# Performance work log

Hardware: AMD Instinct MI355X
Metric: run time of the kernel (lower is better)

Reference implementation:

```python
import jax, jax.numpy as jnp
import numpy as np

HIDDEN = 1024
HEADS = 16
HEAD_DIM = HIDDEN // HEADS


def setup_inputs() -> dict:
    key = jax.random.key(0)
    ks = jax.random.split(key, 7)
    B, S = 2, 2048
    scale = 1.0 / np.sqrt(HIDDEN)
    return {
        "hidden_states": jax.random.normal(ks[0], (B, S, HIDDEN), dtype=jnp.float32),
        "attention_mask": jnp.zeros((B, S), dtype=jnp.float32),
        "Wq": jax.random.normal(ks[1], (HIDDEN, HIDDEN), dtype=jnp.float32) * scale,
        "bq": jnp.zeros((HIDDEN,), dtype=jnp.float32),
        "Wk": jax.random.normal(ks[2], (HIDDEN, HIDDEN), dtype=jnp.float32) * scale,
        "bk": jnp.zeros((HIDDEN,), dtype=jnp.float32),
        "Wv": jax.random.normal(ks[3], (HIDDEN, HIDDEN), dtype=jnp.float32) * scale,
        "bv": jnp.zeros((HIDDEN,), dtype=jnp.float32),
    }


def reference(hidden_states, attention_mask, Wq, bq, Wk, bk, Wv, bv):
    B, S, _ = hidden_states.shape
    def heads(x):  # [B,S,HIDDEN] -> [B,H,S,D]
        return x.reshape(B, S, HEADS, HEAD_DIM).transpose(0, 2, 1, 3)
    q = heads(hidden_states @ Wq + bq)
    k = heads(hidden_states @ Wk + bk)
    v = heads(hidden_states @ Wv + bv)
    scores = jnp.einsum('bhqd,bhkd->bhqk', q, k) / np.sqrt(HEAD_DIM).astype(np.float32)
    # additive mask broadcast [B,1,1,S]
    scores = scores + attention_mask[:, None, None, :]
    probs = jax.nn.softmax(scores, axis=-1)
    # dropout is identity in eval mode (reference baseline)
    ctx = jnp.einsum('bhqk,bhkd->bhqd', probs, v)
    return ctx.transpose(0, 2, 1, 3).reshape(B, S, HIDDEN)
```

## Files before the change

### kernel.cpp

```cpp
#include <hip/hip_runtime.h>
#include <cstdint>
#include <cstddef>

typedef __bf16 bf16;
typedef _Float16 f16;
typedef __attribute__((ext_vector_type(8))) __bf16 bf16x8;
typedef __attribute__((ext_vector_type(4))) float f32x4;
typedef __attribute__((ext_vector_type(16))) float f32x16;
typedef __attribute__((ext_vector_type(4))) _Float16 f16x4;
typedef __attribute__((ext_vector_type(8))) _Float16 f16x8;
typedef __attribute__((ext_vector_type(4))) short short4v;

#define MFMA16(a, b, c) __builtin_amdgcn_mfma_f32_16x16x32_bf16((a), (b), (c), 0, 0, 0)
#define MFMA32(a, b, c) __builtin_amdgcn_mfma_f32_32x32x16_bf16((a), (b), (c), 0, 0, 0)

static constexpr int BB   = 2;
static constexpr int SS   = 2048;
static constexpr int HID  = 1024;
static constexpr int NH   = 16;
static constexpr int HD   = 64;
static constexpr int MROW = BB * SS;
static constexpr int NQKV = 3 * HID;
static constexpr float LOG2E = 1.4426950408889634f;
static constexpr float MSHIFT = 16.0f;

__device__ __forceinline__ int SW(int r) { return ((r ^ (r >> 3)) & 7) << 4; }

__device__ __forceinline__ uint32_t pack_bf16(float a, float b) {
    union { bf16 h[2]; uint32_t u; } x;
    x.h[0] = (bf16)a; x.h[1] = (bf16)b;
    return x.u;
}

__device__ __forceinline__ float exp2i(float x) {
    float r; asm("v_exp_f32 %0, %1" : "=v"(r) : "v"(x)); return r;
}

__device__ __forceinline__ void plswap(uint32_t& a, uint32_t& b) {
    asm("v_permlane32_swap_b32 %0, %1" : "+v"(a), "+v"(b));
}

__device__ __forceinline__ void gload16(const void* g, void* l) {
    __builtin_amdgcn_global_load_lds(
        (const __attribute__((address_space(1))) void*)g,
        (__attribute__((address_space(3))) void*)l, 16, 0, 0);
}

__global__ __launch_bounds__(256) void cvt_hidden(const float* __restrict__ in,
                                                  bf16* __restrict__ out) {
    const int i = (blockIdx.x * 256 + threadIdx.x) * 8;
    float4 f0 = *(const float4*)&in[i];
    float4 f1 = *(const float4*)&in[i + 4];
    bf16x8 o;
    o[0] = (bf16)f0.x; o[1] = (bf16)f0.y; o[2] = (bf16)f0.z; o[3] = (bf16)f0.w;
    o[4] = (bf16)f1.x; o[5] = (bf16)f1.y; o[6] = (bf16)f1.z; o[7] = (bf16)f1.w;
    *(bf16x8*)&out[i] = o;
}

__global__ __launch_bounds__(256) void maskcvt(const float* __restrict__ m,
                                               float* __restrict__ o) {
    const int i = blockIdx.x * 256 + threadIdx.x;
    o[i] = m[i] * LOG2E - MSHIFT;
}

__global__ __launch_bounds__(256) void wtrans(const float* __restrict__ Wq,
                                              const float* __restrict__ Wk,
                                              const float* __restrict__ Wv,
                                              bf16* __restrict__ Wt) {
    __shared__ float tile[32][33];
    const float* W = (blockIdx.z == 0) ? Wq : (blockIdx.z == 1) ? Wk : Wv;
    bf16* O = Wt + (size_t)blockIdx.z * HID * HID;
    const int x  = blockIdx.x * 32 + threadIdx.x;
    const int y0 = blockIdx.y * 32;
#pragma unroll
    for (int i = threadIdx.y; i < 32; i += 8)
        tile[i][threadIdx.x] = W[(size_t)(y0 + i) * HID + x];
    __syncthreads();
    const int k = y0 + threadIdx.x;
#pragma unroll
    for (int i = threadIdx.y; i < 32; i += 8)
        O[(size_t)(blockIdx.x * 32 + i) * HID + k] = (bf16)tile[threadIdx.x][i];
}

__global__ __launch_bounds__(256) void qkv_gemm(
    const bf16* __restrict__ A, const bf16* __restrict__ Bt,
    const float* __restrict__ bq, const float* __restrict__ bk,
    const float* __restrict__ bv,
    bf16* __restrict__ Qo, bf16* __restrict__ Ko, bf16* __restrict__ Vo) {
    __shared__ __align__(16) bf16 As[128 * 32];
    __shared__ __align__(16) bf16 Bs[128 * 32];
    const int t = threadIdx.x, l = t & 63;
    const int l15 = l & 15, l4 = l >> 4;
    const int w = t >> 6;
    const int wm = w >> 1, wn = w & 1;
    const int m0 = blockIdx.y * 128, n0 = blockIdx.x * 128;

    f32x4 acc[4][4] = {};

    for (int kt = 0; kt < 32; ++kt) {
        const int k0 = kt * 32;
        __syncthreads();
#pragma unroll
        for (int cc = 0; cc < 2; ++cc) {
            const int c = t + cc * 256;
            const int row = c >> 2, col = (c & 3) * 8;
            gload16(&A[(size_t)(m0 + row) * HID + k0 + col], (char*)As + c * 16);
            gload16(&Bt[(size_t)(n0 + row) * HID + k0 + col], (char*)Bs + c * 16);
        }
        __syncthreads();

        bf16x8 af[4], bf_[4];
#pragma unroll
        for (int mi = 0; mi < 4; ++mi) {
            const int r = wm * 64 + mi * 16 + l15;
            af[mi] = *(const bf16x8*)((const char*)As + r * 64 + l4 * 16);
        }
#pragma unroll
        for (int ni = 0; ni < 4; ++ni) {
            const int r = wn * 64 + ni * 16 + l15;
            bf_[ni] = *(const bf16x8*)((const char*)Bs + r * 64 + l4 * 16);
        }
        __builtin_amdgcn_s_setprio(1);
#pragma unroll
        for (int mi = 0; mi < 4; ++mi)
#pragma unroll
            for (int ni = 0; ni < 4; ++ni)
                acc[mi][ni] = MFMA16(af[mi], bf_[ni], acc[mi][ni]);
        __builtin_amdgcn_s_setprio(0);
    }

#pragma unroll
    for (int mi = 0; mi < 4; ++mi) {
#pragma unroll
        for (int ni = 0; ni < 4; ++ni) {
            const int ng = n0 + wn * 64 + ni * 16 + l15;
            const int qkv = ng >> 10;
            const int nn = ng & 1023;
            const int hh = nn >> 6, dd = nn & 63;
            const int mg = m0 + wm * 64 + mi * 16 + l4 * 4;
            const int bb = mg >> 11, ss = mg & 2047;
            if (qkv == 2) {
                const float bias = bv[nn];
                union { bf16 h[4]; short4v s4; } pk_;
#pragma unroll
                for (int j = 0; j < 4; ++j)
                    pk_.h[j] = (bf16)(acc[mi][ni][j] + bias);
                bf16* dst = Vo + ((size_t)(bb * NH + hh) * HD + dd) * SS + ss;
                *(short4v*)dst = pk_.s4;
            } else {
                const float* bp = (qkv == 0) ? bq : bk;
                bf16* op = (qkv == 0) ? Qo : Ko;
                const float bias = bp[nn];
                const float scl = (qkv == 0) ? 0.125f * LOG2E : 1.0f;
                bf16* dst = op + ((size_t)(bb * NH + hh) * SS + ss) * HD + dd;
#pragma unroll
                for (int j = 0; j < 4; ++j)
                    dst[(size_t)j * HD] = (bf16)((acc[mi][ni][j] + bias) * scl);
            }
        }
    }
}

__global__ __launch_bounds__(256) void attn_fwd(
    const bf16* __restrict__ Q, const bf16* __restrict__ K,
    const bf16* __restrict__ Vt_g, const float* __restrict__ mkl,
    f16* __restrict__ Op, float* __restrict__ ml) {
    __shared__ __align__(16) char Ks0[64 * 128];
    __shared__ __align__(16) char Ks1[64 * 128];
    __shared__ __align__(16) char Vt0[64 * 128];
    __shared__ __align__(16) char Vt1[64 * 128];

    const int t = threadIdx.x, l = t & 63, w = t >> 6;
    const int l31 = l & 31, h = l >> 5;

    const int bid = blockIdx.x;
    const int nid = (bid & 7) * 128 + (bid >> 3);
    const int bh = nid >> 5, kh = (nid >> 4) & 1, qb = nid & 15;
    const int q0 = qb * 128 + w * 32;
    const int kbase = kh * (SS / 2);

    const bf16* Qp  = Q + (size_t)bh * SS * HD;
    const bf16* Kp  = K + (size_t)bh * SS * HD;
    const bf16* Vpt = Vt_g + (size_t)bh * HD * SS;
    const float* mkp = mkl + (bh >> 4) * SS;

    bf16x8 qf[4];
#pragma unroll
    for (int c = 0; c < 4; ++c)
        qf[c] = *(const bf16x8*)&Qp[(size_t)(q0 + l31) * HD + c * 16 + h * 8];

    float lrun = 0.f;
    f32x16 o0 = {}, o1 = {};

    auto stageK = [&](int tile, char* dst) {
        const int key0 = kbase + tile * 64;
#pragma unroll
        for (int cc = 0; cc < 2; ++cc) {
            const int c = t + cc * 256;
            const int row = c >> 3;
            const int csw = (c & 7) ^ ((row ^ (row >> 3)) & 7);
            gload16(&Kp[(size_t)(key0 + row) * HD + csw * 8], dst + c * 16);
        }
    };
    auto stageVt = [&](int tile, char* dst) {
        const int key0 = kbase + tile * 64;
#pragma unroll
        for (int cc = 0; cc < 2; ++cc) {
            const int c = t + cc * 256;
            const int row = c >> 3;
            const int csw = (c & 7) ^ ((row ^ (row >> 3)) & 7);
            gload16(&Vpt[(size_t)row * SS + key0 + csw * 8], dst + c * 16);
        }
    };

    stageK(0, Ks0);
    stageVt(0, Vt0);
    __syncthreads();

    constexpr int NT = (SS / 2) / 64;
#pragma unroll 1
    for (int kt = 0; kt < NT; ++kt) {
        char* Ks = (kt & 1) ? Ks1 : Ks0;
        char* Vt = (kt & 1) ? Vt1 : Vt0;
        char* Ksn = (kt & 1) ? Ks0 : Ks1;
        char* Vtn = (kt & 1) ? Vt0 : Vt1;
        const int key0 = kbase + kt * 64;
        const bool more = (kt + 1) < NT;

        if (more) {
            stageK(kt + 1, Ksn);
            stageVt(kt + 1, Vtn);
        }

        f32x16 s0, s1;
#pragma unroll
        for (int rq = 0; rq < 4; ++rq) {
            const f32x4 m0v = *(const f32x4*)&mkp[key0 + rq * 8 + 4 * h];
            const f32x4 m1v = *(const f32x4*)&mkp[key0 + 32 + rq * 8 + 4 * h];
#pragma unroll
            for (int j = 0; j < 4; ++j) {
                s0[rq * 4 + j] = m0v[j];
                s1[rq * 4 + j] = m1v[j];
            }
        }
        __builtin_amdgcn_s_setprio(1);
#pragma unroll
        for (int c = 0; c < 4; ++c) {
            const int r0 = l31;
            bf16x8 kf0 = *(const bf16x8*)(Ks + r0 * 128 +
                                          ((c * 32 + h * 16) ^ SW(r0)));
            s0 = MFMA32(kf0, qf[c], s0);
        }
#pragma unroll
        for (int c = 0; c < 4; ++c) {
            const int r1 = 32 + l31;
            bf16x8 kf1 = *(const bf16x8*)(Ks + r1 * 128 +
                                          ((c * 32 + h * 16) ^ SW(r1)));
            s1 = MFMA32(kf1, qf[c], s1);
        }
        __builtin_amdgcn_s_setprio(0);

#pragma unroll
        for (int g = 0; g < 2; ++g) {
            f32x16& st = g ? s1 : s0;
            float ps = 0.f;
#pragma unroll
            for (int r = 0; r < 16; ++r) {
                const float p = exp2i(st[r]);
                st[r] = p;
                ps += p;
            }
            lrun += ps;
#pragma unroll
            for (int cc = 0; cc < 2; ++cc) {
                uint32_t wA = pack_bf16(st[8 * cc + 0], st[8 * cc + 1]);
                uint32_t wB = pack_bf16(st[8 * cc + 2], st[8 * cc + 3]);
                uint32_t wC = pack_bf16(st[8 * cc + 4], st[8 * cc + 5]);
                uint32_t wD = pack_bf16(st[8 * cc + 6], st[8 * cc + 7]);
                plswap(wA, wC);
                plswap(wB, wD);
                union { uint32_t u[4]; bf16x8 v; } pb;
                pb.u[0] = wA; pb.u[1] = wB; pb.u[2] = wC; pb.u[3] = wD;
                const int colb = g * 64 + cc * 32 + h * 16;
                __builtin_amdgcn_s_setprio(1);
                {
                    bf16x8 vf0 = *(const bf16x8*)(Vt + l31 * 128 +
                                                  (colb ^ SW(l31)));
                    o0 = MFMA32(vf0, pb.v, o0);
                    const int r1 = 32 + l31;
                    bf16x8 vf1 = *(const bf16x8*)(Vt + r1 * 128 +
                                                  (colb ^ SW(r1)));
                    o1 = MFMA32(vf1, pb.v, o1);
                }
                __builtin_amdgcn_s_setprio(0);
            }
        }
        __syncthreads();
    }

    lrun += __shfl_xor(lrun, 32);
    const int part = kh * 512 + bh * 16 + qb;
    f16* Ob = Op + (size_t)part * 8192;
    const int row = w * 32 + l31;
#pragma unroll
    for (int rq = 0; rq < 4; ++rq) {
        f16x4 a, b2;
#pragma unroll
        for (int j = 0; j < 4; ++j) {
            a[j]  = (f16)o0[rq * 4 + j];
            b2[j] = (f16)o1[rq * 4 + j];
        }
        *(f16x4*)&Ob[row * 64 + rq * 8 + 4 * h] = a;
        *(f16x4*)&Ob[row * 64 + 32 + rq * 8 + 4 * h] = b2;
    }
    if (l < 32) ml[(size_t)part * 128 + (w * 32 + l)] = lrun;
}

__global__ __launch_bounds__(256) void combine(
    const f16* __restrict__ Op, const float* __restrict__ ml,
    float* __restrict__ out) {
    const int tid = blockIdx.x * 256 + threadIdx.x;
    const int dg = tid & 7, gq = tid >> 3;
    const int bh = gq >> 11, s = gq & 2047;
    const int qb = s >> 7, q = s & 127;
    const int p0 = bh * 16 + qb, p1 = 512 + p0;

    const float l1 = ml[(size_t)p0 * 128 + q];
    const float l2 = ml[(size_t)p1 * 128 + q];
    const float inv = 1.0f / (l1 + l2);

    const f16x8 O1 = *(const f16x8*)&Op[(size_t)p0 * 8192 + q * 64 + dg * 8];
    const f16x8 O2 = *(const f16x8*)&Op[(size_t)p1 * 8192 + q * 64 + dg * 8];
    f32x4 r0, r1;
#pragma unroll
    for (int i = 0; i < 4; ++i) {
        r0[i] = ((float)O1[i] + (float)O2[i]) * inv;
        r1[i] = ((float)O1[4 + i] + (float)O2[4 + i]) * inv;
    }

    const int b = bh >> 4, hh = bh & 15;
    float* op = &out[((size_t)(b * SS + s)) * HID + hh * HD + dg * 8];
    *(f32x4*)op = r0;
    *(f32x4*)(op + 4) = r1;
}

extern "C" void kernel_launch(void* const* d_in, const int* in_sizes, int n_in,
                              void* d_out, int out_size, void* d_ws, size_t ws_size,
                              hipStream_t stream) {
    (void)in_sizes; (void)n_in; (void)out_size; (void)ws_size;
    const float* hs  = (const float*)d_in[0];
    const float* msk = (const float*)d_in[1];
    const float* Wq  = (const float*)d_in[2];
    const float* bq  = (const float*)d_in[3];
    const float* Wk  = (const float*)d_in[4];
    const float* bk  = (const float*)d_in[5];
    const float* Wv  = (const float*)d_in[6];
    const float* bv  = (const float*)d_in[7];
    float* out = (float*)d_out;
    char* ws = (char*)d_ws;
    const size_t MB = 1 << 20;

    bf16* Qb  = (bf16*)ws;
    bf16* Kb  = (bf16*)(ws + 8 * MB);
    bf16* Vb  = (bf16*)(ws + 16 * MB);
    float* mk2 = (float*)(ws + 24 * MB);
    bf16* Xb  = (bf16*)(ws + 25 * MB);
    bf16* Wt  = (bf16*)(ws + 33 * MB);
    f16* Opp  = (f16*)(ws + 25 * MB);
    float* mlp = (float*)(ws + 59 * MB);

    cvt_hidden<<<dim3(MROW * HID / (256 * 8)), dim3(256), 0, stream>>>(hs, Xb);
    maskcvt<<<dim3(BB * SS / 256), dim3(256), 0, stream>>>(msk, mk2);
    wtrans<<<dim3(32, 32, 3), dim3(32, 8), 0, stream>>>(Wq, Wk, Wv, Wt);
    qkv_gemm<<<dim3(NQKV / 128, MROW / 128), dim3(256), 0, stream>>>(
        Xb, Wt, bq, bk, bv, Qb, Kb, Vb);
    attn_fwd<<<dim3(1024), dim3(256), 0, stream>>>(Qb, Kb, Vb, mk2, Opp, mlp);
    combine<<<dim3(2048), dim3(256), 0, stream>>>(Opp, mlp, out);
}
```

Baseline: 119.6 us.

## Drop split-K attention and combine kernel; write normalized output directly via LDS

The attention kernel no longer splits keys into two halves with a separate combine pass. Each block processes the full key range, normalizes by the row sum, and stages the fp32 output through swizzled shared memory for coalesced global stores. This removes the f16 partial writes, the readback and one kernel launch. The QKV GEMM also gets a remapped 1D grid that groups blocks across XCDs for L2 locality. In exchange, attention runs only 512 blocks, half as many, so parallelism on 256 CUs drops and each block's serial loop doubles.

```diff
diff --git a/kernel.cpp b/kernel.cpp
--- a/kernel.cpp
+++ b/kernel.cpp
@@ -3,12 +3,9 @@
 #include <cstddef>
 
 typedef __bf16 bf16;
-typedef _Float16 f16;
 typedef __attribute__((ext_vector_type(8))) __bf16 bf16x8;
 typedef __attribute__((ext_vector_type(4))) float f32x4;
 typedef __attribute__((ext_vector_type(16))) float f32x16;
-typedef __attribute__((ext_vector_type(4))) _Float16 f16x4;
-typedef __attribute__((ext_vector_type(8))) _Float16 f16x8;
 typedef __attribute__((ext_vector_type(4))) short short4v;
 
 #define MFMA16(a, b, c) __builtin_amdgcn_mfma_f32_16x16x32_bf16((a), (b), (c), 0, 0, 0)
@@ -93,7 +90,11 @@
     const int l15 = l & 15, l4 = l >> 4;
     const int w = t >> 6;
     const int wm = w >> 1, wn = w & 1;
-    const int m0 = blockIdx.y * 128, n0 = blockIdx.x * 128;
+
+    const int bid = blockIdx.x;
+    const int nid = (bid & 7) * 96 + (bid >> 3);
+    const int m0 = (nid & 31) * 128;
+    const int n0 = (nid >> 5) * 128;
 
     f32x4 acc[4][4] = {};
 
@@ -164,25 +165,22 @@
 __global__ __launch_bounds__(256) void attn_fwd(
     const bf16* __restrict__ Q, const bf16* __restrict__ K,
     const bf16* __restrict__ Vt_g, const float* __restrict__ mkl,
-    f16* __restrict__ Op, float* __restrict__ ml) {
-    __shared__ __align__(16) char Ks0[64 * 128];
-    __shared__ __align__(16) char Ks1[64 * 128];
-    __shared__ __align__(16) char Vt0[64 * 128];
-    __shared__ __align__(16) char Vt1[64 * 128];
+    float* __restrict__ out) {
+    __shared__ __align__(16) char smem[32768];
 
     const int t = threadIdx.x, l = t & 63, w = t >> 6;
     const int l31 = l & 31, h = l >> 5;
 
     const int bid = blockIdx.x;
-    const int nid = (bid & 7) * 128 + (bid >> 3);
-    const int bh = nid >> 5, kh = (nid >> 4) & 1, qb = nid & 15;
+    const int nid = (bid & 7) * 64 + (bid >> 3);
+    const int bh = nid >> 4, qb = nid & 15;
+    const int b = bh >> 4, hh = bh & 15;
     const int q0 = qb * 128 + w * 32;
-    const int kbase = kh * (SS / 2);
 
     const bf16* Qp  = Q + (size_t)bh * SS * HD;
     const bf16* Kp  = K + (size_t)bh * SS * HD;
     const bf16* Vpt = Vt_g + (size_t)bh * HD * SS;
-    const float* mkp = mkl + (bh >> 4) * SS;
+    const float* mkp = mkl + b * SS;
 
     bf16x8 qf[4];
 #pragma unroll
@@ -193,7 +191,7 @@
     f32x16 o0 = {}, o1 = {};
 
     auto stageK = [&](int tile, char* dst) {
-        const int key0 = kbase + tile * 64;
+        const int key0 = tile * 64;
 #pragma unroll
         for (int cc = 0; cc < 2; ++cc) {
             const int c = t + cc * 256;
@@ -203,7 +201,7 @@
         }
     };
     auto stageVt = [&](int tile, char* dst) {
-        const int key0 = kbase + tile * 64;
+        const int key0 = tile * 64;
 #pragma unroll
         for (int cc = 0; cc < 2; ++cc) {
             const int c = t + cc * 256;
@@ -213,18 +211,18 @@
         }
     };
 
-    stageK(0, Ks0);
-    stageVt(0, Vt0);
+    stageK(0, smem);
+    stageVt(0, smem + 16384);
     __syncthreads();
 
-    constexpr int NT = (SS / 2) / 64;
+    constexpr int NT = SS / 64;
 #pragma unroll 1
     for (int kt = 0; kt < NT; ++kt) {
-        char* Ks = (kt & 1) ? Ks1 : Ks0;
-        char* Vt = (kt & 1) ? Vt1 : Vt0;
-        char* Ksn = (kt & 1) ? Ks0 : Ks1;
-        char* Vtn = (kt & 1) ? Vt0 : Vt1;
-        const int key0 = kbase + kt * 64;
+        char* Ks  = smem + (kt & 1) * 8192;
+        char* Vt  = smem + 16384 + (kt & 1) * 8192;
+        char* Ksn = smem + ((kt + 1) & 1) * 8192;
+        char* Vtn = smem + 16384 + ((kt + 1) & 1) * 8192;
+        const int key0 = kt * 64;
         const bool more = (kt + 1) < NT;
 
         if (more) {
@@ -299,49 +297,29 @@
     }
 
     lrun += __shfl_xor(lrun, 32);
-    const int part = kh * 512 + bh * 16 + qb;
-    f16* Ob = Op + (size_t)part * 8192;
-    const int row = w * 32 + l31;
-#pragma unroll
-    for (int rq = 0; rq < 4; ++rq) {
-        f16x4 a, b2;
+    const float inv = 1.0f / lrun;
+    char* myB = smem + w * 8192;
+#pragma unroll
+    for (int r4 = 0; r4 < 4; ++r4) {
+        f32x4 a, b2;
 #pragma unroll
         for (int j = 0; j < 4; ++j) {
-            a[j]  = (f16)o0[rq * 4 + j];
-            b2[j] = (f16)o1[rq * 4 + j];
-        }
-        *(f16x4*)&Ob[row * 64 + rq * 8 + 4 * h] = a;
-        *(f16x4*)&Ob[row * 64 + 32 + rq * 8 + 4 * h] = b2;
-    }
-    if (l < 32) ml[(size_t)part * 128 + (w * 32 + l)] = lrun;
-}
-
-__global__ __launch_bounds__(256) void combine(
-    const f16* __restrict__ Op, const float* __restrict__ ml,
-    float* __restrict__ out) {
-    const int tid = blockIdx.x * 256 + threadIdx.x;
-    const int dg = tid & 7, gq = tid >> 3;
-    const int bh = gq >> 11, s = gq & 2047;
-    const int qb = s >> 7, q = s & 127;
-    const int p0 = bh * 16 + qb, p1 = 512 + p0;
-
-    const float l1 = ml[(size_t)p0 * 128 + q];
-    const float l2 = ml[(size_t)p1 * 128 + q];
-    const float inv = 1.0f / (l1 + l2);
-
-    const f16x8 O1 = *(const f16x8*)&Op[(size_t)p0 * 8192 + q * 64 + dg * 8];
-    const f16x8 O2 = *(const f16x8*)&Op[(size_t)p1 * 8192 + q * 64 + dg * 8];
-    f32x4 r0, r1;
-#pragma unroll
-    for (int i = 0; i < 4; ++i) {
-        r0[i] = ((float)O1[i] + (float)O2[i]) * inv;
-        r1[i] = ((float)O1[4 + i] + (float)O2[4 + i]) * inv;
-    }
-
-    const int b = bh >> 4, hh = bh & 15;
-    float* op = &out[((size_t)(b * SS + s)) * HID + hh * HD + dg * 8];
-    *(f32x4*)op = r0;
-    *(f32x4*)(op + 4) = r1;
+            a[j]  = o0[r4 * 4 + j] * inv;
+            b2[j] = o1[r4 * 4 + j] * inv;
+        }
+        const int s0_ = 2 * r4 + h;
+        const int s1_ = 8 + 2 * r4 + h;
+        *(f32x4*)(myB + l31 * 256 + ((s0_ ^ (l31 & 15)) * 16)) = a;
+        *(f32x4*)(myB + l31 * 256 + ((s1_ ^ (l31 & 15)) * 16)) = b2;
+    }
+    const int qr = l >> 1, halfd = l & 1;
+    float* op = &out[((size_t)(b * SS) + q0 + qr) * HID + hh * HD + halfd * 32];
+#pragma unroll
+    for (int s = 0; s < 8; ++s) {
+        const int slot = halfd * 8 + s;
+        f32x4 v = *(const f32x4*)(myB + qr * 256 + ((slot ^ (qr & 15)) * 16));
+        *(f32x4*)(op + s * 4) = v;
+    }
 }
 
 extern "C" void kernel_launch(void* const* d_in, const int* in_sizes, int n_in,
@@ -366,14 +344,11 @@
     float* mk2 = (float*)(ws + 24 * MB);
     bf16* Xb  = (bf16*)(ws + 25 * MB);
     bf16* Wt  = (bf16*)(ws + 33 * MB);
-    f16* Opp  = (f16*)(ws + 25 * MB);
-    float* mlp = (float*)(ws + 59 * MB);
 
     cvt_hidden<<<dim3(MROW * HID / (256 * 8)), dim3(256), 0, stream>>>(hs, Xb);
     maskcvt<<<dim3(BB * SS / 256), dim3(256), 0, stream>>>(msk, mk2);
     wtrans<<<dim3(32, 32, 3), dim3(32, 8), 0, stream>>>(Wq, Wk, Wv, Wt);
-    qkv_gemm<<<dim3(NQKV / 128, MROW / 128), dim3(256), 0, stream>>>(
+    qkv_gemm<<<dim3(768), dim3(256), 0, stream>>>(
         Xb, Wt, bq, bk, bv, Qb, Kb, Vb);
-    attn_fwd<<<dim3(1024), dim3(256), 0, stream>>>(Qb, Kb, Vb, mk2, Opp, mlp);
-    combine<<<dim3(2048), dim3(256), 0, stream>>>(Opp, mlp, out);
-}
+    attn_fwd<<<dim3(512), dim3(256), 0, stream>>>(Qb, Kb, Vb, mk2, out);
+}
```

After: 114.7 us. 1.04x faster.
